# Optimization experiments

Hardware: AMD Instinct MI355X
Metric: run time of the kernel (lower is better)

Reference implementation:

```python
import jax, jax.numpy as jnp
import numpy as np

B, T, C = 2, 2048, 2048
NUM_HEADS, NUM_KV_HEADS, HEAD_DIM = 16, 4, 128
ROPE_THETA = 10000.0
SOFTCAP = 50.0


def sine_table(features, length, min_timescale=1.0, max_timescale=10000.0):
    fraction = jnp.arange(0, features, 2, dtype=jnp.float32) / features
    timescale = min_timescale * (max_timescale / min_timescale) ** fraction
    sinusoid = jnp.arange(length, dtype=jnp.float32)[:, None] / timescale[None, :]
    sinusoid = jnp.concatenate([sinusoid, sinusoid], axis=-1)
    return jnp.sin(sinusoid), jnp.cos(sinusoid)


def rotate_half(x):
    x1, x2 = jnp.split(x, 2, axis=-1)
    return jnp.concatenate([-x2, x1], axis=-1)


def setup_inputs() -> dict:
    key = jax.random.key(0)
    k1, k2, k3, k4, k5 = jax.random.split(key, 5)
    x = jax.random.normal(k1, (B, T, C), dtype=jnp.float32)
    mask = jnp.tril(jnp.ones((T, T), dtype=bool))[None, None]  # causal [1,1,T,T]
    mask = jnp.broadcast_to(mask, (B, 1, T, T))
    std = 0.02
    q_kernel = std * jax.random.normal(k2, (C, NUM_HEADS * HEAD_DIM), dtype=jnp.float32)
    k_kernel = std * jax.random.normal(k3, (C, NUM_KV_HEADS * HEAD_DIM), dtype=jnp.float32)
    v_kernel = std * jax.random.normal(k4, (C, NUM_KV_HEADS * HEAD_DIM), dtype=jnp.float32)
    out_kernel = std * jax.random.normal(k5, (NUM_HEADS * HEAD_DIM, C), dtype=jnp.float32)
    return {"x": x, "mask": mask, "q_kernel": q_kernel, "k_kernel": k_kernel,
            "v_kernel": v_kernel, "out_kernel": out_kernel}


def reference(x, mask, q_kernel, k_kernel, v_kernel, out_kernel):
    _, t, c = x.shape
    r = NUM_HEADS // NUM_KV_HEADS  # GQA group size
    qp = q_kernel.reshape(c, r, NUM_KV_HEADS, HEAD_DIM)
    kp = k_kernel.reshape(c, NUM_KV_HEADS, HEAD_DIM)
    vp = v_kernel.reshape(c, NUM_KV_HEADS, HEAD_DIM)
    op = out_kernel.reshape(r, NUM_KV_HEADS, HEAD_DIM, c)
    q = jnp.einsum('bsm,mrhk->brhsk', x, qp)   # [B,r,h,T,hd]
    k = jnp.einsum('bdm,mhk->bhdk', x, kp)     # [B,h,T,hd]
    v = jnp.einsum('bdm,mhv->bhdv', x, vp)     # [B,h,T,hd]
    sin, cos = sine_table(HEAD_DIM, t, max_timescale=ROPE_THETA)  # [T,hd]
    q = q * cos + rotate_half(q) * sin  # broadcast over leading dims (time at -2)
    k = k * cos + rotate_half(k) * sin
    scale = jax.lax.rsqrt(jnp.array(HEAD_DIM, dtype=x.dtype))
    qk = jnp.einsum('brhsk,bhdk->brhsd', q, k) * scale  # [B,r,h,T,T]
    qk = jnp.tanh(qk / SOFTCAP) * SOFTCAP  # logit softcap
    m = jnp.expand_dims(mask, axis=1)  # [B,1,1,T,T]
    qk = jax.nn.softmax(qk.astype(jnp.float32), where=m).astype(x.dtype)
    qkv = jnp.einsum('brhsd,bhdv->brhsv', qk, v)
    out = jnp.einsum('brhsv,rhvm->bsm', qkv, op)
    return out
```

## Files before the change

### kernel.cpp

```cpp
#include <hip/hip_runtime.h>
#include <hip/hip_bf16.h>

typedef __hip_bfloat16 bf16;
typedef __attribute__((ext_vector_type(8))) short bf16x8;
typedef __attribute__((ext_vector_type(4))) short bf16x4;
typedef __attribute__((ext_vector_type(4))) float f32x4;

#define BATCH 2
#define SEQ 2048
#define CDIM 2048
#define NH 16
#define NKV 4
#define HD 128
#define NQKV 3072

__device__ __forceinline__ float tof(float x)  { return x; }
__device__ __forceinline__ float tof(bf16 x)   { return __bfloat162float(x); }
__device__ __forceinline__ void  stf(float* p, float v) { *p = v; }
__device__ __forceinline__ void  stf(bf16* p,  float v) { *p = __float2bfloat16(v); }

__device__ __forceinline__ void gl_lds16(const bf16* g, bf16* l) {
    typedef const __attribute__((address_space(1))) unsigned int* gp_t;
    typedef __attribute__((address_space(3))) unsigned int* lp_t;
    __builtin_amdgcn_global_load_lds((gp_t)g, (lp_t)l, 16, 0, 0);
}

__device__ __forceinline__ f32x4 mfma16x16x16_bf16(bf16x4 a, bf16x4 b, f32x4 c) {
#if __has_builtin(__builtin_amdgcn_mfma_f32_16x16x16bf16_1k)
    return __builtin_amdgcn_mfma_f32_16x16x16bf16_1k(a, b, c, 0, 0, 0);
#else
    asm volatile("v_mfma_f32_16x16x16_bf16 %0, %1, %2, %0"
                 : "+v"(c) : "v"(a), "v"(b));
    return c;
#endif
}

__device__ __forceinline__ float fast_exp2(float x) {
#if __has_builtin(__builtin_amdgcn_exp2f)
    return __builtin_amdgcn_exp2f(x);
#else
    return exp2f(x);
#endif
}

__device__ __forceinline__ float softcap_exp(float u) {
    float t2 = u * u;
    float w = fmaf(t2, -1.328448e-7f, 0.12753101f);
    return fast_exp2(u * w);
}

__global__ __launch_bounds__(256) void f2b_kernel(const float* __restrict__ in,
                                                  bf16* __restrict__ out, int n4)
{
    int i = blockIdx.x * 256 + threadIdx.x;
    if (i >= n4) return;
    float4 v = *(const float4*)&in[(size_t)i * 4];
    bf16 o[4] = {__float2bfloat16(v.x), __float2bfloat16(v.y),
                 __float2bfloat16(v.z), __float2bfloat16(v.w)};
    *(ushort4*)&out[(size_t)i * 4] = *(ushort4*)o;
}

__global__ __launch_bounds__(256) void transpose_f2b_kernel(
    const float* __restrict__ in, bf16* __restrict__ out, int R, int Cn)
{
    __shared__ float tile[64][65];
    const int r0 = blockIdx.y * 64, c0 = blockIdx.x * 64;
    for (int f = threadIdx.x; f < 4096; f += 256) {
        int r = f >> 6, c = f & 63;
        tile[r][c] = in[(size_t)(r0 + r) * Cn + c0 + c];
    }
    __syncthreads();
    for (int f = threadIdx.x; f < 4096; f += 256) {
        int r = f >> 6, c = f & 63;
        out[(size_t)(c0 + r) * R + r0 + c] = __float2bfloat16(tile[c][r]);
    }
}

__global__ __launch_bounds__(256) void vtrans_kernel(
    const bf16* __restrict__ in, bf16* __restrict__ out)
{
    __shared__ bf16 tile[64][65];
    const int b = blockIdx.z;
    const int t0 = blockIdx.y * 64, c0 = blockIdx.x * 64;
    for (int f = threadIdx.x; f < 4096; f += 256) {
        int r = f >> 6, c = f & 63;
        tile[r][c] = in[(size_t)(b * SEQ + t0 + r) * (NKV * HD) + c0 + c];
    }
    __syncthreads();
    for (int f = threadIdx.x; f < 4096; f += 256) {
        int r = f >> 6, c = f & 63;
        out[(size_t)(b * NKV * HD + c0 + r) * SEQ + t0 + c] = tile[c][r];
    }
}

__global__ __launch_bounds__(256) void gemm_qkv_kernel(
    const bf16* __restrict__ A, const bf16* __restrict__ Bt,
    bf16* __restrict__ Qr, bf16* __restrict__ Kr, bf16* __restrict__ Vr,
    int M, int K)
{
    __shared__ __align__(16) bf16 As[128 * 32];
    __shared__ __align__(16) bf16 Bs[128 * 32];

    const int tid = threadIdx.x;
    const int lane = tid & 63;
    const int wave = tid >> 6;
    const int m0 = blockIdx.y * 128;
    const int n0 = blockIdx.x * 128;
    const int wm = (wave >> 1) * 64;
    const int wn = (wave & 1) * 64;
    const int quad = lane >> 4;
    const int l16 = lane & 15;

    const int srow = tid >> 2;
    const int scol = (tid & 3) * 8;
    const bf16* Ag0 = A  + (size_t)(m0 + srow) * K + scol;
    const bf16* Ag1 = A  + (size_t)(m0 + srow + 64) * K + scol;
    const bf16* Bg0 = Bt + (size_t)(n0 + srow) * K + scol;
    const bf16* Bg1 = Bt + (size_t)(n0 + srow + 64) * K + scol;

    f32x4 acc[4][4];
#pragma unroll
    for (int mi = 0; mi < 4; ++mi)
#pragma unroll
        for (int ni = 0; ni < 4; ++ni)
            acc[mi][ni] = (f32x4){0.f, 0.f, 0.f, 0.f};

    for (int kt = 0; kt < K; kt += 32) {
        __syncthreads();
        gl_lds16(Ag0 + kt, &As[tid * 8]);
        gl_lds16(Ag1 + kt, &As[2048 + tid * 8]);
        gl_lds16(Bg0 + kt, &Bs[tid * 8]);
        gl_lds16(Bg1 + kt, &Bs[2048 + tid * 8]);
        __syncthreads();

        bf16x8 a[4], b[4];
#pragma unroll
        for (int mi = 0; mi < 4; ++mi)
            a[mi] = *(const bf16x8*)&As[(wm + mi * 16 + l16) * 32 + quad * 8];
#pragma unroll
        for (int ni = 0; ni < 4; ++ni)
            b[ni] = *(const bf16x8*)&Bs[(wn + ni * 16 + l16) * 32 + quad * 8];
#pragma unroll
        for (int mi = 0; mi < 4; ++mi)
#pragma unroll
            for (int ni = 0; ni < 4; ++ni)
                acc[mi][ni] = __builtin_amdgcn_mfma_f32_16x16x32_bf16(
                    a[mi], b[ni], acc[mi][ni], 0, 0, 0);
    }

    bf16* Cp; int Nst, cbase;
    if (n0 < 2048)      { Cp = Qr; Nst = 2048; cbase = n0; }
    else if (n0 < 2560) { Cp = Kr; Nst = 512;  cbase = n0 - 2048; }
    else                { Cp = Vr; Nst = 512;  cbase = n0 - 2560; }

#pragma unroll
    for (int mi = 0; mi < 4; ++mi)
#pragma unroll
        for (int ni = 0; ni < 4; ++ni) {
            int col = cbase + wn + ni * 16 + l16;
#pragma unroll
            for (int r = 0; r < 4; ++r) {
                int row = m0 + wm + mi * 16 + quad * 4 + r;
                Cp[(size_t)row * Nst + col] = __float2bfloat16(acc[mi][ni][r]);
            }
        }
}

template <typename TC>
__global__ __launch_bounds__(256) void gemm_mfma_bt(
    const bf16* __restrict__ A, const bf16* __restrict__ Bt, TC* __restrict__ C,
    int M, int N, int K)
{
    __shared__ __align__(16) bf16 As[128 * 32];
    __shared__ __align__(16) bf16 Bs[128 * 32];

    const int tid = threadIdx.x;
    const int lane = tid & 63;
    const int wave = tid >> 6;
    const int m0 = blockIdx.y * 128;
    const int n0 = blockIdx.x * 128;
    const int wm = (wave >> 1) * 64;
    const int wn = (wave & 1) * 64;
    const int quad = lane >> 4;
    const int l16 = lane & 15;

    const int srow = tid >> 2;
    const int scol = (tid & 3) * 8;
    const bf16* Ag0 = A  + (size_t)(m0 + srow) * K + scol;
    const bf16* Ag1 = A  + (size_t)(m0 + srow + 64) * K + scol;
    const bf16* Bg0 = Bt + (size_t)(n0 + srow) * K + scol;
    const bf16* Bg1 = Bt + (size_t)(n0 + srow + 64) * K + scol;

    f32x4 acc[4][4];
#pragma unroll
    for (int mi = 0; mi < 4; ++mi)
#pragma unroll
        for (int ni = 0; ni < 4; ++ni)
            acc[mi][ni] = (f32x4){0.f, 0.f, 0.f, 0.f};

    for (int kt = 0; kt < K; kt += 32) {
        __syncthreads();
        gl_lds16(Ag0 + kt, &As[tid * 8]);
        gl_lds16(Ag1 + kt, &As[2048 + tid * 8]);
        gl_lds16(Bg0 + kt, &Bs[tid * 8]);
        gl_lds16(Bg1 + kt, &Bs[2048 + tid * 8]);
        __syncthreads();

        bf16x8 a[4], b[4];
#pragma unroll
        for (int mi = 0; mi < 4; ++mi)
            a[mi] = *(const bf16x8*)&As[(wm + mi * 16 + l16) * 32 + quad * 8];
#pragma unroll
        for (int ni = 0; ni < 4; ++ni)
            b[ni] = *(const bf16x8*)&Bs[(wn + ni * 16 + l16) * 32 + quad * 8];
#pragma unroll
        for (int mi = 0; mi < 4; ++mi)
#pragma unroll
            for (int ni = 0; ni < 4; ++ni)
                acc[mi][ni] = __builtin_amdgcn_mfma_f32_16x16x32_bf16(
                    a[mi], b[ni], acc[mi][ni], 0, 0, 0);
    }

#pragma unroll
    for (int mi = 0; mi < 4; ++mi)
#pragma unroll
        for (int ni = 0; ni < 4; ++ni) {
            int col = n0 + wn + ni * 16 + l16;
#pragma unroll
            for (int r = 0; r < 4; ++r) {
                int row = m0 + wm + mi * 16 + quad * 4 + r;
                stf(&C[(size_t)row * N + col], acc[mi][ni][r]);
            }
        }
}

__global__ __launch_bounds__(256) void rope_kernel(bf16* __restrict__ data,
                                                   int ncols, int total_pairs)
{
    int idx = blockIdx.x * 256 + threadIdx.x;
    if (idx >= total_pairs) return;
    int half = ncols >> 1;
    int row = idx / half;
    int p = idx - row * half;
    int head = p >> 6;
    int i = p & 63;
    int t = row & (SEQ - 1);
    float inv_ts = expf(-(float)i * 0.14391156831212787f);
    float angle = (float)t * inv_ts;
    float s, c;
    sincosf(angle, &s, &c);
    size_t base = (size_t)row * ncols + head * 128 + i;
    float x1 = __bfloat162float(data[base]);
    float x2 = __bfloat162float(data[base + 64]);
    data[base]      = __float2bfloat16(x1 * c - x2 * s);
    data[base + 64] = __float2bfloat16(x2 * c + x1 * s);
}

template <bool WA>
__device__ __forceinline__ void attn_tile_compute(
    const bf16* __restrict__ Ksr, const bf16* __restrict__ Vtsr,
    const bf16x8 (&qfA)[4], const bf16x8 (&qfB)[4],
    f32x4 (&OA)[8], f32x4 (&OB)[8], float& lsumA, float& lsumB,
    int quad, int l16, bool diagA, bool diagB, int qselA, int qselB)
{
#pragma unroll
    for (int half = 0; half < 2; ++half) {
        f32x4 sA[2], sB[2];
        bf16x4 pfA[2], pfB[2];
#pragma unroll
        for (int mt = 0; mt < 2; ++mt) {
            sB[mt] = (f32x4){0.f, 0.f, 0.f, 0.f};
            if constexpr (WA) sA[mt] = (f32x4){0.f, 0.f, 0.f, 0.f};
            const int krow = (half * 32 + mt * 16 + l16) * 128;
#pragma unroll
            for (int kk = 0; kk < 4; ++kk) {
                bf16x8 kf = *(const bf16x8*)&Ksr[krow + (((kk * 4 + quad) ^ l16) * 8)];
                sB[mt] = __builtin_amdgcn_mfma_f32_16x16x32_bf16(
                    kf, qfB[kk], sB[mt], 0, 0, 0);
                if constexpr (WA)
                    sA[mt] = __builtin_amdgcn_mfma_f32_16x16x32_bf16(
                        kf, qfA[kk], sA[mt], 0, 0, 0);
            }
        }
#pragma unroll
        for (int mt = 0; mt < 2; ++mt) {
            bf16 pb[4];
#pragma unroll
            for (int r = 0; r < 4; ++r) {
                float p = softcap_exp(sB[mt][r]);
                if (diagB) {
                    int kl = half * 32 + mt * 16 + quad * 4 + r;
                    p = (kl <= qselB) ? p : 0.f;
                }
                lsumB += p;
                pb[r] = __float2bfloat16(p);
            }
            pfB[mt] = *(bf16x4*)pb;
            if constexpr (WA) {
                bf16 pa[4];
#pragma unroll
                for (int r = 0; r < 4; ++r) {
                    float p = softcap_exp(sA[mt][r]);
                    if (diagA) {
                        int kl = half * 32 + mt * 16 + quad * 4 + r;
                        p = (kl <= qselA) ? p : 0.f;
                    }
                    lsumA += p;
                    pa[r] = __float2bfloat16(p);
                }
                pfA[mt] = *(bf16x4*)pa;
            }
        }
#pragma unroll
        for (int dj = 0; dj < 8; ++dj) {
            const int vrow = (dj * 16 + l16) * 64;
            const int dl7 = l16 & 7;
#pragma unroll
            for (int mt = 0; mt < 2; ++mt) {
                int c16 = half * 4 + mt * 2 + (quad >> 1);
                bf16x4 vf = *(const bf16x4*)&Vtsr[vrow + ((c16 ^ dl7) << 3)
                                                  + (quad & 1) * 4];
                OB[dj] = mfma16x16x16_bf16(vf, pfB[mt], OB[dj]);
                if constexpr (WA)
                    OA[dj] = mfma16x16x16_bf16(vf, pfA[mt], OA[dj]);
            }
        }
    }
}

__global__ __launch_bounds__(256, 2) void attn_mfma8_kernel(
    const bf16* __restrict__ Q, const bf16* __restrict__ K,
    const bf16* __restrict__ Vt, bf16* __restrict__ Att)
{
    __shared__ __align__(16) char smem[65536];

    const int tid = threadIdx.x;
    const int lane = tid & 63;
    const int w = tid >> 6;
    const int hs = w >> 1;
    const int qw = w & 1;
    const int quad = lane >> 4;
    const int l16 = lane & 15;
    const int bh = blockIdx.y;
    const int b   = bh >> 3;
    const int kvh = (bh >> 1) & 3;
    const int pr  = bh & 1;
    const int hq  = kvh + 4 * (pr * 2 + hs);
    const int qlo = blockIdx.x;
    const int qhi = 63 - qlo;
    const int ntlo = (qlo >> 1) + 1;
    const int nthi = (qhi >> 1) + 1;
    const int q0A = qlo * 32 + qw * 16;
    const int q0B = qhi * 32 + qw * 16;

    bf16x8 qfA[4], qfB[4];
    {
        size_t ra = (size_t)(b * SEQ + q0A + l16) * (NH * HD) + hq * HD;
        size_t rb = (size_t)(b * SEQ + q0B + l16) * (NH * HD) + hq * HD;
#pragma unroll
        for (int kk = 0; kk < 4; ++kk) {
            qfA[kk] = *(const bf16x8*)&Q[ra + kk * 32 + quad * 8];
            qfB[kk] = *(const bf16x8*)&Q[rb + kk * 32 + quad * 8];
        }
    }

    const bf16* Kb = K  + (size_t)(b * SEQ) * (NKV * HD) + kvh * HD;
    const bf16* Vb = Vt + (size_t)((b * NKV + kvh) * HD) * SEQ;

    f32x4 OA[8], OB[8];
#pragma unroll
    for (int dj = 0; dj < 8; ++dj) {
        OA[dj] = (f32x4){0.f, 0.f, 0.f, 0.f};
        OB[dj] = (f32x4){0.f, 0.f, 0.f, 0.f};
    }
    float lsumA = 0.f, lsumB = 0.f;

    const int srowK = tid >> 4;
    const int sgcK  = (tid & 15) ^ srowK;
    const int srowV = tid >> 3;
    const int sgcV  = (tid & 7) ^ (srowV & 7);

    const int qselA = (qlo & 1) * 32 + qw * 16 + l16;
    const int qselB = (qhi & 1) * 32 + qw * 16 + l16;

    {
        bf16* KsW  = (bf16*)smem;
        bf16* VtsW = (bf16*)(smem + 32768);
#pragma unroll
        for (int c = 0; c < 4; ++c) {
            gl_lds16(Kb + (size_t)(c * 16 + srowK) * (NKV * HD) + sgcK * 8,
                     KsW + c * 2048 + tid * 8);
            gl_lds16(Vb + (size_t)(c * 32 + srowV) * SEQ + sgcV * 8,
                     VtsW + c * 2048 + tid * 8);
        }
    }
    __syncthreads();

    int cur = 0;
    for (int jt = 0; jt < nthi; ++jt) {
        if (jt + 1 < nthi) {
            const int j0 = (jt + 1) * 64;
            bf16* KsW  = (bf16*)(smem + (cur ^ 1) * 16384);
            bf16* VtsW = (bf16*)(smem + 32768 + (cur ^ 1) * 16384);
#pragma unroll
            for (int c = 0; c < 4; ++c) {
                gl_lds16(Kb + (size_t)(j0 + c * 16 + srowK) * (NKV * HD) + sgcK * 8,
                         KsW + c * 2048 + tid * 8);
                gl_lds16(Vb + (size_t)(c * 32 + srowV) * SEQ + j0 + sgcV * 8,
                         VtsW + c * 2048 + tid * 8);
            }
        }
        const bf16* Ksr  = (const bf16*)(smem + cur * 16384);
        const bf16* Vtsr = (const bf16*)(smem + 32768 + cur * 16384);
        const bool diagA = (jt == ntlo - 1);
        const bool diagB = (jt == nthi - 1);
        if (jt < ntlo)
            attn_tile_compute<true>(Ksr, Vtsr, qfA, qfB, OA, OB, lsumA, lsumB,
                                    quad, l16, diagA, diagB, qselA, qselB);
        else
            attn_tile_compute<false>(Ksr, Vtsr, qfA, qfB, OA, OB, lsumA, lsumB,
                                     quad, l16, diagA, diagB, qselA, qselB);
        __syncthreads();
        cur ^= 1;
    }

    {
        float v = lsumA;
        v += __shfl_xor(v, 16);
        v += __shfl_xor(v, 32);
        float inv = 1.f / v;
        size_t obase = (size_t)(b * SEQ + q0A + l16) * (NH * HD) + hq * HD;
#pragma unroll
        for (int dj = 0; dj < 8; ++dj) {
            bf16 ob[4];
#pragma unroll
            for (int r = 0; r < 4; ++r)
                ob[r] = __float2bfloat16(OA[dj][r] * inv);
            *(ushort4*)&Att[obase + dj * 16 + quad * 4] = *(ushort4*)ob;
        }
    }
    {
        float v = lsumB;
        v += __shfl_xor(v, 16);
        v += __shfl_xor(v, 32);
        float inv = 1.f / v;
        size_t obase = (size_t)(b * SEQ + q0B + l16) * (NH * HD) + hq * HD;
#pragma unroll
        for (int dj = 0; dj < 8; ++dj) {
            bf16 ob[4];
#pragma unroll
            for (int r = 0; r < 4; ++r)
                ob[r] = __float2bfloat16(OB[dj][r] * inv);
            *(ushort4*)&Att[obase + dj * 16 + quad * 4] = *(ushort4*)ob;
        }
    }
}

extern "C" void kernel_launch(void* const* d_in, const int* in_sizes, int n_in,
                              void* d_out, int out_size, void* d_ws, size_t ws_size,
                              hipStream_t stream) {
    const float* x        = (const float*)d_in[0];
    const float* q_kernel = (const float*)d_in[2];
    const float* k_kernel = (const float*)d_in[3];
    const float* v_kernel = (const float*)d_in[4];
    const float* o_kernel = (const float*)d_in[5];
    float* out = (float*)d_out;

    const int M = BATCH * SEQ;
    char* ws = (char*)d_ws;
    bf16* xb   = (bf16*)ws;
    bf16* Att  = xb;
    bf16* wT   = (bf16*)(ws + 16777216);
    bf16* wTq  = wT;
    bf16* wTk  = wT + (size_t)2048 * 2048;
    bf16* wTv  = wT + (size_t)2560 * 2048;
    bf16* woT  = wT;
    bf16* Vt_g = (bf16*)(ws + 25165824);
    bf16* Qr   = (bf16*)(ws + 29360128);
    bf16* Kr   = (bf16*)(ws + 46137344);
    bf16* Vr   = (bf16*)(ws + 50331648);

    f2b_kernel<<<(M * CDIM / 4 + 255) / 256, 256, 0, stream>>>(x, xb, M * CDIM / 4);
    transpose_f2b_kernel<<<dim3((NH * HD) / 64, CDIM / 64), 256, 0, stream>>>(
        q_kernel, wTq, CDIM, NH * HD);
    transpose_f2b_kernel<<<dim3((NKV * HD) / 64, CDIM / 64), 256, 0, stream>>>(
        k_kernel, wTk, CDIM, NKV * HD);
    transpose_f2b_kernel<<<dim3((NKV * HD) / 64, CDIM / 64), 256, 0, stream>>>(
        v_kernel, wTv, CDIM, NKV * HD);

    gemm_qkv_kernel<<<dim3(NQKV / 128, M / 128), 256, 0, stream>>>(
        xb, wT, Qr, Kr, Vr, M, CDIM);

    transpose_f2b_kernel<<<dim3(CDIM / 64, CDIM / 64), 256, 0, stream>>>(
        o_kernel, woT, CDIM, CDIM);

    {
        int pairs_q = M * (NH * HD / 2);
        rope_kernel<<<pairs_q / 256, 256, 0, stream>>>(Qr, NH * HD, pairs_q);
        int pairs_k = M * (NKV * HD / 2);
        rope_kernel<<<pairs_k / 256, 256, 0, stream>>>(Kr, NKV * HD, pairs_k);
    }

    vtrans_kernel<<<dim3((NKV * HD) / 64, SEQ / 64, BATCH), 256, 0, stream>>>(Vr, Vt_g);

    attn_mfma8_kernel<<<dim3(SEQ / 64, BATCH * NKV * 2), 256, 0, stream>>>(
        Qr, Kr, Vt_g, Att);

    gemm_mfma_bt<float><<<dim3(CDIM / 128, M / 128), 256, 0, stream>>>(
        Att, woT, out, M, CDIM, CDIM);
}
```

Baseline: 370.0 us.

## Split attention key tile across two wave groups with LDS reduction

Doubles the attention block to 512 threads. Each half of the waves processes one 32-key half of every 64-key tile, and partial outputs and row sums are combined through shared memory at the end. Global-to-LDS loads are spread over twice as many threads. The aim is more waves in flight to hide latency, at the cost of an extra reduction pass, larger LDS use and tighter register limits from launch_bounds(512,4).

Result: slower. 772.0 us (+108.7%).

```diff
diff --git a/kernel.cpp b/kernel.cpp
--- a/kernel.cpp
+++ b/kernel.cpp
@@ -261,83 +261,81 @@
     const bf16* __restrict__ Ksr, const bf16* __restrict__ Vtsr,
     const bf16x8 (&qfA)[4], const bf16x8 (&qfB)[4],
     f32x4 (&OA)[8], f32x4 (&OB)[8], float& lsumA, float& lsumB,
-    int quad, int l16, bool diagA, bool diagB, int qselA, int qselB)
-{
-#pragma unroll
-    for (int half = 0; half < 2; ++half) {
-        f32x4 sA[2], sB[2];
-        bf16x4 pfA[2], pfB[2];
+    int quad, int l16, int ks, bool diagA, bool diagB, int qselA, int qselB)
+{
+    f32x4 sA[2], sB[2];
+    bf16x4 pfA[2], pfB[2];
+#pragma unroll
+    for (int mt = 0; mt < 2; ++mt) {
+        sB[mt] = (f32x4){0.f, 0.f, 0.f, 0.f};
+        if constexpr (WA) sA[mt] = (f32x4){0.f, 0.f, 0.f, 0.f};
+        const int krow = (ks * 32 + mt * 16 + l16) * 128;
+#pragma unroll
+        for (int kk = 0; kk < 4; ++kk) {
+            bf16x8 kf = *(const bf16x8*)&Ksr[krow + (((kk * 4 + quad) ^ l16) * 8)];
+            sB[mt] = __builtin_amdgcn_mfma_f32_16x16x32_bf16(
+                kf, qfB[kk], sB[mt], 0, 0, 0);
+            if constexpr (WA)
+                sA[mt] = __builtin_amdgcn_mfma_f32_16x16x32_bf16(
+                    kf, qfA[kk], sA[mt], 0, 0, 0);
+        }
+    }
+#pragma unroll
+    for (int mt = 0; mt < 2; ++mt) {
+        bf16 pb[4];
+#pragma unroll
+        for (int r = 0; r < 4; ++r) {
+            float p = softcap_exp(sB[mt][r]);
+            if (diagB) {
+                int kl = ks * 32 + mt * 16 + quad * 4 + r;
+                p = (kl <= qselB) ? p : 0.f;
+            }
+            lsumB += p;
+            pb[r] = __float2bfloat16(p);
+        }
+        pfB[mt] = *(bf16x4*)pb;
+        if constexpr (WA) {
+            bf16 pa[4];
+#pragma unroll
+            for (int r = 0; r < 4; ++r) {
+                float p = softcap_exp(sA[mt][r]);
+                if (diagA) {
+                    int kl = ks * 32 + mt * 16 + quad * 4 + r;
+                    p = (kl <= qselA) ? p : 0.f;
+                }
+                lsumA += p;
+                pa[r] = __float2bfloat16(p);
+            }
+            pfA[mt] = *(bf16x4*)pa;
+        }
+    }
+#pragma unroll
+    for (int dj = 0; dj < 8; ++dj) {
+        const int vrow = (dj * 16 + l16) * 64;
+        const int dl7 = l16 & 7;
 #pragma unroll
         for (int mt = 0; mt < 2; ++mt) {
-            sB[mt] = (f32x4){0.f, 0.f, 0.f, 0.f};
-            if constexpr (WA) sA[mt] = (f32x4){0.f, 0.f, 0.f, 0.f};
-            const int krow = (half * 32 + mt * 16 + l16) * 128;
-#pragma unroll
-            for (int kk = 0; kk < 4; ++kk) {
-                bf16x8 kf = *(const bf16x8*)&Ksr[krow + (((kk * 4 + quad) ^ l16) * 8)];
-                sB[mt] = __builtin_amdgcn_mfma_f32_16x16x32_bf16(
-                    kf, qfB[kk], sB[mt], 0, 0, 0);
-                if constexpr (WA)
-                    sA[mt] = __builtin_amdgcn_mfma_f32_16x16x32_bf16(
-                        kf, qfA[kk], sA[mt], 0, 0, 0);
-            }
-        }
-#pragma unroll
-        for (int mt = 0; mt < 2; ++mt) {
-            bf16 pb[4];
-#pragma unroll
-            for (int r = 0; r < 4; ++r) {
-                float p = softcap_exp(sB[mt][r]);
-                if (diagB) {
-                    int kl = half * 32 + mt * 16 + quad * 4 + r;
-                    p = (kl <= qselB) ? p : 0.f;
-                }
-                lsumB += p;
-                pb[r] = __float2bfloat16(p);
-            }
-            pfB[mt] = *(bf16x4*)pb;
-            if constexpr (WA) {
-                bf16 pa[4];
-#pragma unroll
-                for (int r = 0; r < 4; ++r) {
-                    float p = softcap_exp(sA[mt][r]);
-                    if (diagA) {
-                        int kl = half * 32 + mt * 16 + quad * 4 + r;
-                        p = (kl <= qselA) ? p : 0.f;
-                    }
-                    lsumA += p;
-                    pa[r] = __float2bfloat16(p);
-                }
-                pfA[mt] = *(bf16x4*)pa;
-            }
-        }
-#pragma unroll
-        for (int dj = 0; dj < 8; ++dj) {
-            const int vrow = (dj * 16 + l16) * 64;
-            const int dl7 = l16 & 7;
-#pragma unroll
-            for (int mt = 0; mt < 2; ++mt) {
-                int c16 = half * 4 + mt * 2 + (quad >> 1);
-                bf16x4 vf = *(const bf16x4*)&Vtsr[vrow + ((c16 ^ dl7) << 3)
-                                                  + (quad & 1) * 4];
-                OB[dj] = mfma16x16x16_bf16(vf, pfB[mt], OB[dj]);
-                if constexpr (WA)
-                    OA[dj] = mfma16x16x16_bf16(vf, pfA[mt], OA[dj]);
-            }
-        }
-    }
-}
-
-__global__ __launch_bounds__(256, 2) void attn_mfma8_kernel(
+            int c16 = ks * 4 + mt * 2 + (quad >> 1);
+            bf16x4 vf = *(const bf16x4*)&Vtsr[vrow + ((c16 ^ dl7) << 3)
+                                              + (quad & 1) * 4];
+            OB[dj] = mfma16x16x16_bf16(vf, pfB[mt], OB[dj]);
+            if constexpr (WA)
+                OA[dj] = mfma16x16x16_bf16(vf, pfA[mt], OA[dj]);
+        }
+    }
+}
+
+__global__ __launch_bounds__(512, 4) void attn_mfma9_kernel(
     const bf16* __restrict__ Q, const bf16* __restrict__ K,
     const bf16* __restrict__ Vt, bf16* __restrict__ Att)
 {
-    __shared__ __align__(16) char smem[65536];
+    __shared__ __align__(16) char smem[70144];
 
     const int tid = threadIdx.x;
     const int lane = tid & 63;
     const int w = tid >> 6;
-    const int hs = w >> 1;
+    const int ks = w >> 2;
+    const int hs = (w >> 1) & 1;
     const int qw = w & 1;
     const int quad = lane >> 4;
     const int l16 = lane & 15;
@@ -375,24 +373,22 @@
     }
     float lsumA = 0.f, lsumB = 0.f;
 
-    const int srowK = tid >> 4;
-    const int sgcK  = (tid & 15) ^ srowK;
-    const int srowV = tid >> 3;
-    const int sgcV  = (tid & 7) ^ (srowV & 7);
-
     const int qselA = (qlo & 1) * 32 + qw * 16 + l16;
     const int qselB = (qhi & 1) * 32 + qw * 16 + l16;
+
+    const int sK0 = tid, sK1 = 512 + tid;
+    const int keyK0 = sK0 >> 4, chK0 = (sK0 & 15) ^ (keyK0 & 15);
+    const int keyK1 = sK1 >> 4, chK1 = (sK1 & 15) ^ (keyK1 & 15);
+    const int dV0 = sK0 >> 3, chV0 = (sK0 & 7) ^ (dV0 & 7);
+    const int dV1 = sK1 >> 3, chV1 = (sK1 & 7) ^ (dV1 & 7);
 
     {
         bf16* KsW  = (bf16*)smem;
         bf16* VtsW = (bf16*)(smem + 32768);
-#pragma unroll
-        for (int c = 0; c < 4; ++c) {
-            gl_lds16(Kb + (size_t)(c * 16 + srowK) * (NKV * HD) + sgcK * 8,
-                     KsW + c * 2048 + tid * 8);
-            gl_lds16(Vb + (size_t)(c * 32 + srowV) * SEQ + sgcV * 8,
-                     VtsW + c * 2048 + tid * 8);
-        }
+        gl_lds16(Kb + (size_t)keyK0 * (NKV * HD) + chK0 * 8, KsW + sK0 * 8);
+        gl_lds16(Kb + (size_t)keyK1 * (NKV * HD) + chK1 * 8, KsW + sK1 * 8);
+        gl_lds16(Vb + (size_t)dV0 * SEQ + chV0 * 8, VtsW + sK0 * 8);
+        gl_lds16(Vb + (size_t)dV1 * SEQ + chV1 * 8, VtsW + sK1 * 8);
     }
     __syncthreads();
 
@@ -402,13 +398,10 @@
             const int j0 = (jt + 1) * 64;
             bf16* KsW  = (bf16*)(smem + (cur ^ 1) * 16384);
             bf16* VtsW = (bf16*)(smem + 32768 + (cur ^ 1) * 16384);
-#pragma unroll
-            for (int c = 0; c < 4; ++c) {
-                gl_lds16(Kb + (size_t)(j0 + c * 16 + srowK) * (NKV * HD) + sgcK * 8,
-                         KsW + c * 2048 + tid * 8);
-                gl_lds16(Vb + (size_t)(c * 32 + srowV) * SEQ + j0 + sgcV * 8,
-                         VtsW + c * 2048 + tid * 8);
-            }
+            gl_lds16(Kb + (size_t)(j0 + keyK0) * (NKV * HD) + chK0 * 8, KsW + sK0 * 8);
+            gl_lds16(Kb + (size_t)(j0 + keyK1) * (NKV * HD) + chK1 * 8, KsW + sK1 * 8);
+            gl_lds16(Vb + (size_t)dV0 * SEQ + j0 + chV0 * 8, VtsW + sK0 * 8);
+            gl_lds16(Vb + (size_t)dV1 * SEQ + j0 + chV1 * 8, VtsW + sK1 * 8);
         }
         const bf16* Ksr  = (const bf16*)(smem + cur * 16384);
         const bf16* Vtsr = (const bf16*)(smem + 32768 + cur * 16384);
@@ -416,42 +409,70 @@
         const bool diagB = (jt == nthi - 1);
         if (jt < ntlo)
             attn_tile_compute<true>(Ksr, Vtsr, qfA, qfB, OA, OB, lsumA, lsumB,
-                                    quad, l16, diagA, diagB, qselA, qselB);
+                                    quad, l16, ks, diagA, diagB, qselA, qselB);
         else
             attn_tile_compute<false>(Ksr, Vtsr, qfA, qfB, OA, OB, lsumA, lsumB,
-                                     quad, l16, diagA, diagB, qselA, qselB);
+                                     quad, l16, ks, diagA, diagB, qselA, qselB);
         __syncthreads();
         cur ^= 1;
     }
 
-    {
-        float v = lsumA;
-        v += __shfl_xor(v, 16);
-        v += __shfl_xor(v, 32);
-        float inv = 1.f / v;
-        size_t obase = (size_t)(b * SEQ + q0A + l16) * (NH * HD) + hq * HD;
+    float* Osh = (float*)smem;
+    float* Lsh = (float*)(smem + 69632);
+    const int p = hs * 2 + qw;
+    const int ob = (p * 64 + lane) * 68;
+    if (ks == 1) {
 #pragma unroll
         for (int dj = 0; dj < 8; ++dj) {
-            bf16 ob[4];
-#pragma unroll
-            for (int r = 0; r < 4; ++r)
-                ob[r] = __float2bfloat16(OA[dj][r] * inv);
-            *(ushort4*)&Att[obase + dj * 16 + quad * 4] = *(ushort4*)ob;
-        }
-    }
-    {
-        float v = lsumB;
-        v += __shfl_xor(v, 16);
-        v += __shfl_xor(v, 32);
-        float inv = 1.f / v;
-        size_t obase = (size_t)(b * SEQ + q0B + l16) * (NH * HD) + hq * HD;
-#pragma unroll
-        for (int dj = 0; dj < 8; ++dj) {
-            bf16 ob[4];
-#pragma unroll
-            for (int r = 0; r < 4; ++r)
-                ob[r] = __float2bfloat16(OB[dj][r] * inv);
-            *(ushort4*)&Att[obase + dj * 16 + quad * 4] = *(ushort4*)ob;
+            *(f32x4*)&Osh[ob + dj * 4]      = OA[dj];
+            *(f32x4*)&Osh[ob + 32 + dj * 4] = OB[dj];
+        }
+        float vA = lsumA;
+        vA += __shfl_xor(vA, 16);
+        vA += __shfl_xor(vA, 32);
+        float vB = lsumB;
+        vB += __shfl_xor(vB, 16);
+        vB += __shfl_xor(vB, 32);
+        if (quad == 0) {
+            Lsh[p * 32 + l16]      = vA;
+            Lsh[p * 32 + 16 + l16] = vB;
+        }
+    }
+    __syncthreads();
+    if (ks == 0) {
+        {
+            float v = lsumA;
+            v += __shfl_xor(v, 16);
+            v += __shfl_xor(v, 32);
+            v += Lsh[p * 32 + l16];
+            float inv = 1.f / v;
+            size_t obase = (size_t)(b * SEQ + q0A + l16) * (NH * HD) + hq * HD;
+#pragma unroll
+            for (int dj = 0; dj < 8; ++dj) {
+                f32x4 o = OA[dj] + *(const f32x4*)&Osh[ob + dj * 4];
+                bf16 obuf[4];
+#pragma unroll
+                for (int r = 0; r < 4; ++r)
+                    obuf[r] = __float2bfloat16(o[r] * inv);
+                *(ushort4*)&Att[obase + dj * 16 + quad * 4] = *(ushort4*)obuf;
+            }
+        }
+        {
+            float v = lsumB;
+            v += __shfl_xor(v, 16);
+            v += __shfl_xor(v, 32);
+            v += Lsh[p * 32 + 16 + l16];
+            float inv = 1.f / v;
+            size_t obase = (size_t)(b * SEQ + q0B + l16) * (NH * HD) + hq * HD;
+#pragma unroll
+            for (int dj = 0; dj < 8; ++dj) {
+                f32x4 o = OB[dj] + *(const f32x4*)&Osh[ob + 32 + dj * 4];
+                bf16 obuf[4];
+#pragma unroll
+                for (int r = 0; r < 4; ++r)
+                    obuf[r] = __float2bfloat16(o[r] * inv);
+                *(ushort4*)&Att[obase + dj * 16 + quad * 4] = *(ushort4*)obuf;
+            }
         }
     }
 }
@@ -503,7 +524,7 @@
 
     vtrans_kernel<<<dim3((NKV * HD) / 64, SEQ / 64, BATCH), 256, 0, stream>>>(Vr, Vt_g);
 
-    attn_mfma8_kernel<<<dim3(SEQ / 64, BATCH * NKV * 2), 256, 0, stream>>>(
+    attn_mfma9_kernel<<<dim3(SEQ / 64, BATCH * NKV * 2), 512, 0, stream>>>(
         Qr, Kr, Vt_g, Att);
 
     gemm_mfma_bt<float><<<dim3(CDIM / 128, M / 128), 256, 0, stream>>>(
```
